# Optimization experiments

Measured on AMD Instinct MI355X. Metric: run time of the kernel, lower is better.

Reference implementation:

```python
import jax, jax.numpy as jnp
import numpy as np

N_EDGES = 1_600_000
D_FEAT = 32
N_NODES = 50_000


def setup_inputs() -> dict:
    key = jax.random.key(0)
    k1, k2, k3, k4 = jax.random.split(key, 4)
    m = jax.random.normal(k1, (N_EDGES, D_FEAT), dtype=jnp.float32)
    dst = jax.random.randint(k2, (N_EDGES,), 0, N_NODES, dtype=jnp.int64)
    w = jax.random.normal(k3, (4,), dtype=jnp.float32)
    b = jax.random.normal(k4, (1,), dtype=jnp.float32)
    return {"m": m, "dst": dst, "w": w, "b": b, "n_nodes": N_NODES}


def reference(m, dst, w, b, n_nodes):
    # Four segment reductions edge->node over destination index (copy_e_*)
    s = jax.ops.segment_sum(m, dst, num_segments=n_nodes)            # [N, D]
    mn = jax.ops.segment_min(m, dst, num_segments=n_nodes)
    mx = jax.ops.segment_max(m, dst, num_segments=n_nodes)
    deg = jax.ops.segment_sum(jnp.ones((m.shape[0],), m.dtype), dst,
                              num_segments=n_nodes)                  # [N]
    has = (deg > 0)[:, None]
    # DGL returns 0 for zero-degree nodes
    mn = jnp.where(has, mn, 0.0)
    mx = jnp.where(has, mx, 0.0)
    mean = s / jnp.maximum(deg, 1.0)[:, None]
    stacked = jnp.stack([s, mn, mx, mean], axis=-1)                  # [N, D, 4]
    out = jnp.einsum('ndk,k->nd', stacked, w) + b[0]                 # Dense(4,1) + squeeze
    return out
```

## Files before the change

### kernel.cpp

```cpp
#include <hip/hip_runtime.h>
#include <math.h>

#define D_FEAT 32
#define BSHIFT 6
#define NODES_PER_BKT 64
#define TILE 8192
#define PT 32
#define MAXBKT 1024
#define CAP 4096

__global__ void hist_kernel(const int* __restrict__ dst, int* __restrict__ bucketCount,
                            int E4, int nbucket) {
    __shared__ int h[MAXBKT];
    for (int i = threadIdx.x; i < nbucket; i += 256) h[i] = 0;
    __syncthreads();
    const int4* dst4 = (const int4*)dst;
    int tbase4 = blockIdx.x * (TILE / 4);
    #pragma unroll
    for (int k = 0; k < PT / 4; k++) {
        int i4 = tbase4 + k * 256 + threadIdx.x;
        if (i4 < E4) {
            int4 d = dst4[i4];
            atomicAdd(&h[d.x >> BSHIFT], 1);
            atomicAdd(&h[d.y >> BSHIFT], 1);
            atomicAdd(&h[d.z >> BSHIFT], 1);
            atomicAdd(&h[d.w >> BSHIFT], 1);
        }
    }
    __syncthreads();
    for (int i = threadIdx.x; i < nbucket; i += 256) {
        int c = h[i];
        if (c) atomicAdd(&bucketCount[i], c);
    }
}

__global__ void scan_kernel(const int* __restrict__ bucketCount,
                            int* __restrict__ bucketBase, int* __restrict__ bucketCursor,
                            int nbucket, int E) {
    __shared__ int lds[256];
    int tid = threadIdx.x;
    int vals[4];
    int s = 0;
    #pragma unroll
    for (int k = 0; k < 4; k++) {
        int i = tid * 4 + k;
        vals[k] = (i < nbucket) ? bucketCount[i] : 0;
        s += vals[k];
    }
    lds[tid] = s;
    __syncthreads();
    for (int off = 1; off < 256; off <<= 1) {
        int t = (tid >= off) ? lds[tid - off] : 0;
        __syncthreads();
        lds[tid] += t;
        __syncthreads();
    }
    int run = lds[tid] - s;
    #pragma unroll
    for (int k = 0; k < 4; k++) {
        int i = tid * 4 + k;
        if (i < nbucket) { bucketBase[i] = run; bucketCursor[i] = run; }
        run += vals[k];
    }
    if (tid == 0) bucketBase[nbucket] = E;
}

__global__ void partition_kernel(const int* __restrict__ dst,
                                 int* __restrict__ bucketCursor,
                                 unsigned int* __restrict__ keys,
                                 int E4, int nbucket) {
    __shared__ int h[MAXBKT];
    __shared__ int baseL[MAXBKT];
    int tid = threadIdx.x;
    for (int i = tid; i < nbucket; i += 256) h[i] = 0;
    __syncthreads();
    const int4* dst4 = (const int4*)dst;
    int tbase4 = blockIdx.x * (TILE / 4);
    int pk[PT];
    #pragma unroll
    for (int k = 0; k < PT / 4; k++) {
        int i4 = tbase4 + k * 256 + tid;
        if (i4 < E4) {
            int4 d = dst4[i4];
            int b0 = d.x >> BSHIFT; int r0 = atomicAdd(&h[b0], 1);
            int b1 = d.y >> BSHIFT; int r1 = atomicAdd(&h[b1], 1);
            int b2 = d.z >> BSHIFT; int r2 = atomicAdd(&h[b2], 1);
            int b3 = d.w >> BSHIFT; int r3 = atomicAdd(&h[b3], 1);
            pk[4 * k + 0] = (b0 << 19) | ((d.x & 63) << 13) | r0;
            pk[4 * k + 1] = (b1 << 19) | ((d.y & 63) << 13) | r1;
            pk[4 * k + 2] = (b2 << 19) | ((d.z & 63) << 13) | r2;
            pk[4 * k + 3] = (b3 << 19) | ((d.w & 63) << 13) | r3;
        } else {
            pk[4 * k + 0] = -1; pk[4 * k + 1] = -1;
            pk[4 * k + 2] = -1; pk[4 * k + 3] = -1;
        }
    }
    __syncthreads();
    for (int i = tid; i < nbucket; i += 256) {
        int c = h[i];
        baseL[i] = c ? atomicAdd(&bucketCursor[i], c) : 0;
    }
    __syncthreads();
    #pragma unroll
    for (int k = 0; k < PT / 4; k++) {
        int i4 = tbase4 + k * 256 + tid;
        int e = i4 * 4;
        #pragma unroll
        for (int l = 0; l < 4; l++) {
            int p = pk[4 * k + l];
            if (p >= 0) {
                int b   = p >> 19;
                int loc = (p >> 13) & 63;
                int r   = p & 8191;
                keys[baseL[b] + r] = ((unsigned)loc << 26) | (unsigned)(e + l);
            }
        }
    }
}

__global__ __launch_bounds__(256) void bucket_gather_kernel(
        const float* __restrict__ m,
        const unsigned int* __restrict__ keys,
        const int* __restrict__ bucketBase,
        const float* __restrict__ w,
        const float* __restrict__ bia,
        float* __restrict__ out, int N) {
    __shared__ unsigned int ukey[CAP];
    __shared__ int seid[CAP];
    __shared__ int nh[NODES_PER_BKT];
    __shared__ int noff[NODES_PER_BKT + 1];
    __shared__ int ncur[NODES_PER_BKT];
    int bkt = blockIdx.x;
    int tid = threadIdx.x;
    int start = bucketBase[bkt];
    int cnt = bucketBase[bkt + 1] - start;
    if (cnt > CAP) cnt = CAP;

    if (tid < NODES_PER_BKT) nh[tid] = 0;
    __syncthreads();
    for (int i = tid; i < cnt; i += 256) {
        unsigned int k = keys[start + i];
        ukey[i] = k;
        atomicAdd(&nh[k >> 26], 1);
    }
    __syncthreads();
    if (tid < NODES_PER_BKT) {
        int v = nh[tid];
        int x = v;
        #pragma unroll
        for (int off = 1; off < 64; off <<= 1) {
            int t = __shfl_up(x, off, 64);
            if (tid >= off) x += t;
        }
        noff[tid + 1] = x;
        if (tid == 0) noff[0] = 0;
        ncur[tid] = x - v;
    }
    __syncthreads();
    for (int i = tid; i < cnt; i += 256) {
        unsigned int k = ukey[i];
        int pos = atomicAdd(&ncur[k >> 26], 1);
        seid[pos] = (int)(k & 0x03FFFFFFu);
    }
    __syncthreads();

    int hw = tid >> 5;
    int f  = tid & 31;
    int nodeBase = bkt << BSHIFT;
    float w0 = w[0], w1 = w[1], w2 = w[2], w3 = w[3], bb = bia[0];
    for (int nl = hw; nl < NODES_PER_BKT; nl += 8) {
        int node = nodeBase + nl;
        if (node >= N) break;
        int s0 = noff[nl], e0 = noff[nl + 1];
        int deg = e0 - s0;
        float s = 0.0f, mn = INFINITY, mx = -INFINITY;
        int j = s0;
        for (; j + 8 <= e0; j += 8) {
            float v0 = m[seid[j]     * D_FEAT + f];
            float v1 = m[seid[j + 1] * D_FEAT + f];
            float v2 = m[seid[j + 2] * D_FEAT + f];
            float v3 = m[seid[j + 3] * D_FEAT + f];
            float v4 = m[seid[j + 4] * D_FEAT + f];
            float v5 = m[seid[j + 5] * D_FEAT + f];
            float v6 = m[seid[j + 6] * D_FEAT + f];
            float v7 = m[seid[j + 7] * D_FEAT + f];
            s += v0; mn = fminf(mn, v0); mx = fmaxf(mx, v0);
            s += v1; mn = fminf(mn, v1); mx = fmaxf(mx, v1);
            s += v2; mn = fminf(mn, v2); mx = fmaxf(mx, v2);
            s += v3; mn = fminf(mn, v3); mx = fmaxf(mx, v3);
            s += v4; mn = fminf(mn, v4); mx = fmaxf(mx, v4);
            s += v5; mn = fminf(mn, v5); mx = fmaxf(mx, v5);
            s += v6; mn = fminf(mn, v6); mx = fmaxf(mx, v6);
            s += v7; mn = fminf(mn, v7); mx = fmaxf(mx, v7);
        }
        for (; j < e0; j++) {
            float v = m[seid[j] * D_FEAT + f];
            s += v; mn = fminf(mn, v); mx = fmaxf(mx, v);
        }
        bool has = deg > 0;
        float mean = s / fmaxf((float)deg, 1.0f);
        out[node * D_FEAT + f] = w0 * s + w1 * (has ? mn : 0.0f)
                               + w2 * (has ? mx : 0.0f) + w3 * mean + bb;
    }
}

extern "C" void kernel_launch(void* const* d_in, const int* in_sizes, int n_in,
                              void* d_out, int out_size, void* d_ws, size_t ws_size,
                              hipStream_t stream) {
    const float* m   = (const float*)d_in[0];
    const int*   dst = (const int*)  d_in[1];
    const float* w   = (const float*)d_in[2];
    const float* b   = (const float*)d_in[3];

    int E = in_sizes[0] / D_FEAT;
    int N = out_size    / D_FEAT;
    int E4 = E / 4;
    int nbucket = (N + NODES_PER_BKT - 1) >> BSHIFT;

    int* ws           = (int*)d_ws;
    int* bucketCount  = ws;
    int* bucketBase   = bucketCount + MAXBKT;
    int* bucketCursor = bucketBase + MAXBKT + 1;
    unsigned int* keys = (unsigned int*)(bucketCursor + MAXBKT);

    int nTiles = (E + TILE - 1) / TILE;

    hipMemsetAsync(bucketCount, 0, MAXBKT * sizeof(int), stream);
    hipLaunchKernelGGL(hist_kernel, dim3(nTiles), dim3(256), 0, stream,
                       dst, bucketCount, E4, nbucket);
    hipLaunchKernelGGL(scan_kernel, dim3(1), dim3(256), 0, stream,
                       bucketCount, bucketBase, bucketCursor, nbucket, E);
    hipLaunchKernelGGL(partition_kernel, dim3(nTiles), dim3(256), 0, stream,
                       dst, bucketCursor, keys, E4, nbucket);
    hipLaunchKernelGGL(bucket_gather_kernel, dim3(nbucket), dim3(256), 0, stream,
                       m, keys, bucketBase, w, b, (float*)d_out, N);
}
```

Before: 338.1 us.

## Replace per-node sort in gather with LDS atomic accumulation over smaller buckets

The final kernel no longer sorts each bucket's edges by node in shared memory. Each half-warp streams 32 keys, broadcasts them with shuffles, and accumulates sum, min and max into per-node LDS arrays using atomics, with min and max applied to order-preserving unsigned encodings of the floats. Buckets shrink to 32 nodes, giving about 1563 blocks for more parallelism, and the scan is widened to match. This removes the two-pass LDS counting sort and the CAP truncation, at the cost of many LDS atomics, including float atomicAdd. That makes the summation order nondeterministic.

Measured after the change: 572.0 us. 1.69x slower.

```diff
diff --git a/kernel.cpp b/kernel.cpp
--- a/kernel.cpp
+++ b/kernel.cpp
@@ -2,12 +2,20 @@
 #include <math.h>
 
 #define D_FEAT 32
-#define BSHIFT 6
-#define NODES_PER_BKT 64
+#define BSHIFT 5
+#define NODES_PER_BKT 32
 #define TILE 8192
 #define PT 32
-#define MAXBKT 1024
-#define CAP 4096
+#define MAXBKT 2048
+
+__device__ __forceinline__ unsigned mapf(float v) {
+    int b = __float_as_int(v);
+    return (unsigned)(b ^ ((b >> 31) | 0x80000000));
+}
+__device__ __forceinline__ float unmapf(unsigned u) {
+    int b = (u & 0x80000000u) ? (int)(u ^ 0x80000000u) : (int)(~u);
+    return __int_as_float(b);
+}
 
 __global__ void hist_kernel(const int* __restrict__ dst, int* __restrict__ bucketCount,
                             int E4, int nbucket) {
@@ -39,11 +47,11 @@
                             int nbucket, int E) {
     __shared__ int lds[256];
     int tid = threadIdx.x;
-    int vals[4];
+    int vals[8];
     int s = 0;
     #pragma unroll
-    for (int k = 0; k < 4; k++) {
-        int i = tid * 4 + k;
+    for (int k = 0; k < 8; k++) {
+        int i = tid * 8 + k;
         vals[k] = (i < nbucket) ? bucketCount[i] : 0;
         s += vals[k];
     }
@@ -57,8 +65,8 @@
     }
     int run = lds[tid] - s;
     #pragma unroll
-    for (int k = 0; k < 4; k++) {
-        int i = tid * 4 + k;
+    for (int k = 0; k < 8; k++) {
+        int i = tid * 8 + k;
         if (i < nbucket) { bucketBase[i] = run; bucketCursor[i] = run; }
         run += vals[k];
     }
@@ -86,10 +94,10 @@
             int b1 = d.y >> BSHIFT; int r1 = atomicAdd(&h[b1], 1);
             int b2 = d.z >> BSHIFT; int r2 = atomicAdd(&h[b2], 1);
             int b3 = d.w >> BSHIFT; int r3 = atomicAdd(&h[b3], 1);
-            pk[4 * k + 0] = (b0 << 19) | ((d.x & 63) << 13) | r0;
-            pk[4 * k + 1] = (b1 << 19) | ((d.y & 63) << 13) | r1;
-            pk[4 * k + 2] = (b2 << 19) | ((d.z & 63) << 13) | r2;
-            pk[4 * k + 3] = (b3 << 19) | ((d.w & 63) << 13) | r3;
+            pk[4 * k + 0] = (b0 << 18) | ((d.x & (NODES_PER_BKT - 1)) << 13) | r0;
+            pk[4 * k + 1] = (b1 << 18) | ((d.y & (NODES_PER_BKT - 1)) << 13) | r1;
+            pk[4 * k + 2] = (b2 << 18) | ((d.z & (NODES_PER_BKT - 1)) << 13) | r2;
+            pk[4 * k + 3] = (b3 << 18) | ((d.w & (NODES_PER_BKT - 1)) << 13) | r3;
         } else {
             pk[4 * k + 0] = -1; pk[4 * k + 1] = -1;
             pk[4 * k + 2] = -1; pk[4 * k + 3] = -1;
@@ -109,8 +117,8 @@
         for (int l = 0; l < 4; l++) {
             int p = pk[4 * k + l];
             if (p >= 0) {
-                int b   = p >> 19;
-                int loc = (p >> 13) & 63;
+                int b   = p >> 18;
+                int loc = (p >> 13) & (NODES_PER_BKT - 1);
                 int r   = p & 8191;
                 keys[baseL[b] + r] = ((unsigned)loc << 26) | (unsigned)(e + l);
             }
@@ -118,89 +126,82 @@
     }
 }
 
-__global__ __launch_bounds__(256) void bucket_gather_kernel(
+__global__ __launch_bounds__(256) void bucket_acc_kernel(
         const float* __restrict__ m,
         const unsigned int* __restrict__ keys,
         const int* __restrict__ bucketBase,
         const float* __restrict__ w,
         const float* __restrict__ bia,
         float* __restrict__ out, int N) {
-    __shared__ unsigned int ukey[CAP];
-    __shared__ int seid[CAP];
-    __shared__ int nh[NODES_PER_BKT];
-    __shared__ int noff[NODES_PER_BKT + 1];
-    __shared__ int ncur[NODES_PER_BKT];
+    __shared__ float    sSum[NODES_PER_BKT * D_FEAT];
+    __shared__ unsigned sMin[NODES_PER_BKT * D_FEAT];
+    __shared__ unsigned sMax[NODES_PER_BKT * D_FEAT];
+    __shared__ int      sDeg[NODES_PER_BKT];
+    int tid = threadIdx.x;
     int bkt = blockIdx.x;
-    int tid = threadIdx.x;
     int start = bucketBase[bkt];
-    int cnt = bucketBase[bkt + 1] - start;
-    if (cnt > CAP) cnt = CAP;
-
-    if (tid < NODES_PER_BKT) nh[tid] = 0;
-    __syncthreads();
-    for (int i = tid; i < cnt; i += 256) {
-        unsigned int k = keys[start + i];
-        ukey[i] = k;
-        atomicAdd(&nh[k >> 26], 1);
-    }
-    __syncthreads();
-    if (tid < NODES_PER_BKT) {
-        int v = nh[tid];
-        int x = v;
-        #pragma unroll
-        for (int off = 1; off < 64; off <<= 1) {
-            int t = __shfl_up(x, off, 64);
-            if (tid >= off) x += t;
-        }
-        noff[tid + 1] = x;
-        if (tid == 0) noff[0] = 0;
-        ncur[tid] = x - v;
-    }
-    __syncthreads();
-    for (int i = tid; i < cnt; i += 256) {
-        unsigned int k = ukey[i];
-        int pos = atomicAdd(&ncur[k >> 26], 1);
-        seid[pos] = (int)(k & 0x03FFFFFFu);
-    }
+    int cnt   = bucketBase[bkt + 1] - start;
+
+    for (int i = tid; i < NODES_PER_BKT * D_FEAT; i += 256) {
+        sSum[i] = 0.0f;
+        sMin[i] = 0xFFFFFFFFu;
+        sMax[i] = 0u;
+    }
+    if (tid < NODES_PER_BKT) sDeg[tid] = 0;
     __syncthreads();
 
     int hw = tid >> 5;
     int f  = tid & 31;
+
+    for (int g = hw * 32; g < cnt; g += 8 * 32) {
+        int c32 = cnt - g; if (c32 > 32) c32 = 32;
+        int kreg = (f < c32) ? (int)keys[start + g + f] : 0;
+        int j = 0;
+        for (; j + 8 <= c32; j += 8) {
+            float v[8]; int nd[8];
+            #pragma unroll
+            for (int t = 0; t < 8; t++) {
+                unsigned kk = (unsigned)__shfl(kreg, j + t, 32);
+                nd[t] = (int)(kk >> 26);
+                v[t]  = m[(kk & 0x03FFFFFFu) * D_FEAT + f];
+            }
+            #pragma unroll
+            for (int t = 0; t < 8; t++) {
+                int a = nd[t] * D_FEAT + f;
+                atomicAdd(&sSum[a], v[t]);
+                unsigned u = mapf(v[t]);
+                atomicMin(&sMin[a], u);
+                atomicMax(&sMax[a], u);
+                if (f == 0) atomicAdd(&sDeg[nd[t]], 1);
+            }
+        }
+        for (; j < c32; j++) {
+            unsigned kk = (unsigned)__shfl(kreg, j, 32);
+            int node = (int)(kk >> 26);
+            float vv = m[(kk & 0x03FFFFFFu) * D_FEAT + f];
+            int a = node * D_FEAT + f;
+            atomicAdd(&sSum[a], vv);
+            unsigned u = mapf(vv);
+            atomicMin(&sMin[a], u);
+            atomicMax(&sMax[a], u);
+            if (f == 0) atomicAdd(&sDeg[node], 1);
+        }
+    }
+    __syncthreads();
+
+    float w0 = w[0], w1 = w[1], w2 = w[2], w3 = w[3], bb = bia[0];
     int nodeBase = bkt << BSHIFT;
-    float w0 = w[0], w1 = w[1], w2 = w[2], w3 = w[3], bb = bia[0];
-    for (int nl = hw; nl < NODES_PER_BKT; nl += 8) {
+    for (int i = tid; i < NODES_PER_BKT * D_FEAT; i += 256) {
+        int nl = i >> 5;
         int node = nodeBase + nl;
         if (node >= N) break;
-        int s0 = noff[nl], e0 = noff[nl + 1];
-        int deg = e0 - s0;
-        float s = 0.0f, mn = INFINITY, mx = -INFINITY;
-        int j = s0;
-        for (; j + 8 <= e0; j += 8) {
-            float v0 = m[seid[j]     * D_FEAT + f];
-            float v1 = m[seid[j + 1] * D_FEAT + f];
-            float v2 = m[seid[j + 2] * D_FEAT + f];
-            float v3 = m[seid[j + 3] * D_FEAT + f];
-            float v4 = m[seid[j + 4] * D_FEAT + f];
-            float v5 = m[seid[j + 5] * D_FEAT + f];
-            float v6 = m[seid[j + 6] * D_FEAT + f];
-            float v7 = m[seid[j + 7] * D_FEAT + f];
-            s += v0; mn = fminf(mn, v0); mx = fmaxf(mx, v0);
-            s += v1; mn = fminf(mn, v1); mx = fmaxf(mx, v1);
-            s += v2; mn = fminf(mn, v2); mx = fmaxf(mx, v2);
-            s += v3; mn = fminf(mn, v3); mx = fmaxf(mx, v3);
-            s += v4; mn = fminf(mn, v4); mx = fmaxf(mx, v4);
-            s += v5; mn = fminf(mn, v5); mx = fmaxf(mx, v5);
-            s += v6; mn = fminf(mn, v6); mx = fmaxf(mx, v6);
-            s += v7; mn = fminf(mn, v7); mx = fmaxf(mx, v7);
-        }
-        for (; j < e0; j++) {
-            float v = m[seid[j] * D_FEAT + f];
-            s += v; mn = fminf(mn, v); mx = fmaxf(mx, v);
-        }
+        int deg = sDeg[nl];
         bool has = deg > 0;
+        float s = sSum[i];
+        float mnv = has ? unmapf(sMin[i]) : 0.0f;
+        float mxv = has ? unmapf(sMax[i]) : 0.0f;
         float mean = s / fmaxf((float)deg, 1.0f);
-        out[node * D_FEAT + f] = w0 * s + w1 * (has ? mn : 0.0f)
-                               + w2 * (has ? mx : 0.0f) + w3 * mean + bb;
+        out[node * D_FEAT + (i & 31)] = w0 * s + w1 * mnv + w2 * mxv + w3 * mean + bb;
     }
 }
 
@@ -232,6 +233,6 @@
                        bucketCount, bucketBase, bucketCursor, nbucket, E);
     hipLaunchKernelGGL(partition_kernel, dim3(nTiles), dim3(256), 0, stream,
                        dst, bucketCursor, keys, E4, nbucket);
-    hipLaunchKernelGGL(bucket_gather_kernel, dim3(nbucket), dim3(256), 0, stream,
+    hipLaunchKernelGGL(bucket_acc_kernel, dim3(nbucket), dim3(256), 0, stream,
                        m, keys, bucketBase, w, b, (float*)d_out, N);
 }
```
